# Performance work log

Hardware: AMD Instinct MI355X
Metric: run time of the kernel (lower is better)

## Reference

```python
import jax, jax.numpy as jnp
import numpy as np

N = 30000       # mesh nodes
E = 150000      # mesh edges
L = 128         # latent_size
STEPS = 5       # message_passing_steps
TW = 5          # time_window
TD = 2          # target_dim
NODE_IN = TD + 1 + 9   # u + load + node_type one-hot = 12
EDGE_IN = 2 + 1 + TD   # rel_mesh + dist + grad_u = 5


def _mlp(x, W1, b1, W2, b2, g, be):
    # Linear -> ReLU -> Linear -> ReLU -> LayerNorm (matches MLP module)
    h = jax.nn.relu(x @ W1 + b1)
    h = jax.nn.relu(h @ W2 + b2)
    mu = jnp.mean(h, axis=-1, keepdims=True)
    var = jnp.mean(jnp.square(h - mu), axis=-1, keepdims=True)
    return g * (h - mu) / jnp.sqrt(var + 1e-5) + be


def setup_inputs() -> dict:
    key = jax.random.key(0)
    ks = iter(jax.random.split(key, 64))
    def nrm(shape, s=0.05):
        return jax.random.normal(next(ks), shape, dtype=jnp.float32) * s
    inp = {}
    inp['mesh_pos'] = jax.random.normal(next(ks), (1, N, 2), dtype=jnp.float32)
    inp['node_type'] = jax.random.normal(next(ks), (1, N, 9), dtype=jnp.float32)
    inp['u'] = jax.random.normal(next(ks), (1, N, TD), dtype=jnp.float32)
    inp['load'] = jax.random.normal(next(ks), (1, N, 1), dtype=jnp.float32)
    inp['senders'] = jax.random.randint(next(ks), (E,), 0, N, dtype=jnp.int32)
    inp['receivers'] = jax.random.randint(next(ks), (E,), 0, N, dtype=jnp.int32)
    # node encoder MLP(12 -> 128)
    inp['enc_node_W1'] = nrm((NODE_IN, L)); inp['enc_node_b1'] = nrm((L,), 0.01)
    inp['enc_node_W2'] = nrm((L, L));       inp['enc_node_b2'] = nrm((L,), 0.01)
    inp['enc_node_g'] = jnp.ones((L,), jnp.float32); inp['enc_node_be'] = jnp.zeros((L,), jnp.float32)
    # edge encoder MLP(5 -> 128)
    inp['enc_edge_W1'] = nrm((EDGE_IN, L)); inp['enc_edge_b1'] = nrm((L,), 0.01)
    inp['enc_edge_W2'] = nrm((L, L));       inp['enc_edge_b2'] = nrm((L,), 0.01)
    inp['enc_edge_g'] = jnp.ones((L,), jnp.float32); inp['enc_edge_be'] = jnp.zeros((L,), jnp.float32)
    # STEPS GraphNetBlocks, params stacked along leading axis for lax.scan
    inp['blk_edge_W1'] = nrm((STEPS, 3 * L, L)); inp['blk_edge_b1'] = nrm((STEPS, L), 0.01)
    inp['blk_edge_W2'] = nrm((STEPS, L, L));     inp['blk_edge_b2'] = nrm((STEPS, L), 0.01)
    inp['blk_edge_g'] = jnp.ones((STEPS, L), jnp.float32); inp['blk_edge_be'] = jnp.zeros((STEPS, L), jnp.float32)
    inp['blk_node_W1'] = nrm((STEPS, 2 * L, L)); inp['blk_node_b1'] = nrm((STEPS, L), 0.01)
    inp['blk_node_W2'] = nrm((STEPS, L, L));     inp['blk_node_b2'] = nrm((STEPS, L), 0.01)
    inp['blk_node_g'] = jnp.ones((STEPS, L), jnp.float32); inp['blk_node_be'] = jnp.zeros((STEPS, L), jnp.float32)
    # decoder: Conv1d(L,8,1) -> Swish -> Conv1d(8, TD*TW, 1); kernel-size-1 conv == per-node linear
    inp['dec_W1'] = nrm((L, 8)); inp['dec_b1'] = nrm((8,), 0.01)
    inp['dec_W2'] = nrm((8, TD * TW)); inp['dec_b2'] = nrm((TD * TW,), 0.01)
    return inp


def reference(mesh_pos, node_type, u, load, senders, receivers,
              enc_node_W1, enc_node_b1, enc_node_W2, enc_node_b2, enc_node_g, enc_node_be,
              enc_edge_W1, enc_edge_b1, enc_edge_W2, enc_edge_b2, enc_edge_g, enc_edge_be,
              blk_edge_W1, blk_edge_b1, blk_edge_W2, blk_edge_b2, blk_edge_g, blk_edge_be,
              blk_node_W1, blk_node_b1, blk_node_W2, blk_node_b2, blk_node_g, blk_node_be,
              dec_W1, dec_b1, dec_W2, dec_b2):
    # --- encode ---
    node_feats = jnp.concatenate([u, load, node_type], axis=-1)        # [1,N,12]
    nl = _mlp(node_feats, enc_node_W1, enc_node_b1, enc_node_W2, enc_node_b2, enc_node_g, enc_node_be)
    rel = mesh_pos[:, senders] - mesh_pos[:, receivers]                # [1,E,2]
    dist = jnp.linalg.norm(rel, axis=-1, keepdims=True)                # [1,E,1]
    grad_u = u[:, senders] - u[:, receivers]                           # [1,E,2]
    ef = jnp.concatenate([rel, dist, grad_u], axis=-1)                 # [1,E,5]
    el = _mlp(ef, enc_edge_W1, enc_edge_b1, enc_edge_W2, enc_edge_b2, enc_edge_g, enc_edge_be)
    n_nodes = nl.shape[1]

    # --- process: GraphNetBlocks with residual connections ---
    def block(carry, p):
        nl, el = carry
        edge_in = jnp.concatenate([nl[:, senders], nl[:, receivers], el], axis=-1)  # [1,E,3L]
        ne = _mlp(edge_in, p['eW1'], p['eb1'], p['eW2'], p['eb2'], p['eg'], p['ebe'])
        aggr = jax.vmap(lambda e: jax.ops.segment_sum(e, receivers, num_segments=n_nodes))(ne)  # [1,N,L]
        node_in = jnp.concatenate([nl, aggr], axis=-1)                 # [1,N,2L]
        nn = _mlp(node_in, p['nW1'], p['nb1'], p['nW2'], p['nb2'], p['ng'], p['nbe'])
        return (nl + nn, el + ne), None

    ps = {'eW1': blk_edge_W1, 'eb1': blk_edge_b1, 'eW2': blk_edge_W2, 'eb2': blk_edge_b2,
          'eg': blk_edge_g, 'ebe': blk_edge_be,
          'nW1': blk_node_W1, 'nb1': blk_node_b1, 'nW2': blk_node_W2, 'nb2': blk_node_b2,
          'ng': blk_node_g, 'nbe': blk_node_be}
    (nl, el), _ = jax.lax.scan(block, (nl, el), ps)

    # --- decode (1x1 Conv1d == per-node linear) ---
    h = nl @ dec_W1 + dec_b1
    h = h * jax.nn.sigmoid(h)                                          # Swish(beta=1)
    decoded = h @ dec_W2 + dec_b2                                      # [1,N,TW*TD]
    dt = jnp.repeat(jnp.arange(1, TW + 1, dtype=decoded.dtype), TD)    # [TW*TD]
    delta = (decoded * dt).reshape(-1, TW, TD).transpose(1, 0, 2)      # [TW,N,TD]
    return delta
```

## Files before the change

### kernel.cpp

```cpp
#include <hip/hip_runtime.h>
#include <hip/hip_bf16.h>

#define LNUM 128
#define NNODES 30000
#define NEDGES 150000
#define NSTEPS 5


typedef _Float16 f16;
typedef __attribute__((ext_vector_type(8))) _Float16 f16x8;
typedef __attribute__((ext_vector_type(4))) float f32x4;

__device__ __forceinline__ void glds16(const void* g, void* l) {
    __builtin_amdgcn_global_load_lds(
        (const __attribute__((address_space(1))) void*)g,
        (__attribute__((address_space(3))) void*)l, 16, 0, 0);
}

template<int ROWS, int K, int KP>
__device__ __forceinline__ void mlp_apply(
    const float* __restrict__ xs, float* __restrict__ hv,
    float* __restrict__ mu_s, float* __restrict__ rs_s,
    const float* __restrict__ W1, const float* __restrict__ b1,
    const float* __restrict__ W2, const float* __restrict__ b2,
    const float* __restrict__ g,  const float* __restrict__ be,
    float out[ROWS])
{
    const int t = threadIdx.x;
    float acc[ROWS];
    {
        const float bb = b1[t];
        #pragma unroll
        for (int r = 0; r < ROWS; r++) acc[r] = bb;
    }
    int k = 0;
    for (; k + 4 <= K; k += 4) {
        const float w0 = W1[(k + 0) * LNUM + t];
        const float w1 = W1[(k + 1) * LNUM + t];
        const float w2 = W1[(k + 2) * LNUM + t];
        const float w3 = W1[(k + 3) * LNUM + t];
        #pragma unroll
        for (int r = 0; r < ROWS; r++) {
            const float4 x = *(const float4*)(xs + r * KP + k);
            acc[r] = fmaf(x.x, w0, acc[r]);
            acc[r] = fmaf(x.y, w1, acc[r]);
            acc[r] = fmaf(x.z, w2, acc[r]);
            acc[r] = fmaf(x.w, w3, acc[r]);
        }
    }
    for (; k < K; ++k) {
        const float w = W1[k * LNUM + t];
        #pragma unroll
        for (int r = 0; r < ROWS; r++) acc[r] = fmaf(xs[r * KP + k], w, acc[r]);
    }
    #pragma unroll
    for (int r = 0; r < ROWS; r++) hv[r * LNUM + t] = fmaxf(acc[r], 0.f);
    __syncthreads();
    {
        const float bb = b2[t];
        #pragma unroll
        for (int r = 0; r < ROWS; r++) acc[r] = bb;
    }
    for (int k2 = 0; k2 < LNUM; k2 += 4) {
        const float w0 = W2[(k2 + 0) * LNUM + t];
        const float w1 = W2[(k2 + 1) * LNUM + t];
        const float w2 = W2[(k2 + 2) * LNUM + t];
        const float w3 = W2[(k2 + 3) * LNUM + t];
        #pragma unroll
        for (int r = 0; r < ROWS; r++) {
            const float4 x = *(const float4*)(hv + r * LNUM + k2);
            acc[r] = fmaf(x.x, w0, acc[r]);
            acc[r] = fmaf(x.y, w1, acc[r]);
            acc[r] = fmaf(x.z, w2, acc[r]);
            acc[r] = fmaf(x.w, w3, acc[r]);
        }
    }
    __syncthreads();
    #pragma unroll
    for (int r = 0; r < ROWS; r++) hv[r * LNUM + t] = fmaxf(acc[r], 0.f);
    __syncthreads();
    if (t < ROWS) {
        float s = 0.f, s2 = 0.f;
        for (int kk = 0; kk < LNUM; kk++) {
            const float v = hv[t * LNUM + kk];
            s += v; s2 += v * v;
        }
        const float m = s * (1.0f / LNUM);
        mu_s[t] = m;
        rs_s[t] = rsqrtf(fmaxf(s2 * (1.0f / LNUM) - m * m, 0.f) + 1e-5f);
    }
    __syncthreads();
    const float gg = g[t], bbe = be[t];
    #pragma unroll
    for (int r = 0; r < ROWS; r++)
        out[r] = fmaf(gg * (hv[r * LNUM + t] - mu_s[r]), rs_s[r], bbe);
}

__global__ __launch_bounds__(128) void encode_nodes_k(
    const float* __restrict__ u, const float* __restrict__ load_,
    const float* __restrict__ ntype,
    const float* __restrict__ W1, const float* __restrict__ b1,
    const float* __restrict__ W2, const float* __restrict__ b2,
    const float* __restrict__ g,  const float* __restrict__ be,
    float* __restrict__ nl)
{
    constexpr int ROWS = 4, K = 12, KP = 12;
    __shared__ __align__(16) float xs[ROWS * KP];
    __shared__ __align__(16) float hv[ROWS * LNUM];
    __shared__ float mu_s[ROWS], rs_s[ROWS];
    const int t = threadIdx.x;
    const int base = blockIdx.x * ROWS;
    if (t < ROWS * K) {
        const int r = t / K, k = t % K;
        const int n = base + r;
        float v;
        if (k < 2)      v = u[n * 2 + k];
        else if (k < 3) v = load_[n];
        else            v = ntype[n * 9 + (k - 3)];
        xs[r * KP + k] = v;
    }
    __syncthreads();
    float out[ROWS];
    mlp_apply<ROWS, K, KP>(xs, hv, mu_s, rs_s, W1, b1, W2, b2, g, be, out);
    #pragma unroll
    for (int r = 0; r < ROWS; r++) nl[(base + r) * LNUM + t] = out[r];
}

#define PE1 245760
#define PE2 81920
#define PN1 163840
#define PN2 81920
#define PQ1 4096
#define PQ2 16384
#define PTOT (PE1+PE2+PN1+PN2+PQ1+PQ2)

__global__ __launch_bounds__(256) void prep_w_all_k(
    const float* __restrict__ eW1, const float* __restrict__ eW2,
    const float* __restrict__ nW1, const float* __restrict__ nW2,
    const float* __restrict__ qW1, const float* __restrict__ qW2,
    f16* __restrict__ out)
{
    int j = blockIdx.x * 256 + threadIdx.x;
    if (j >= PTOT) return;
    const float* W; int K, kreal; f16* hi; f16* p = out;
    if (j < PE1) { W = eW1; K = 384; kreal = 384; hi = p; }
    else { p += PE1; j -= PE1;
    if (j < PE2) { W = eW2; K = 128; kreal = 128; hi = p; }
    else { p += PE2; j -= PE2;
    if (j < PN1) { W = nW1; K = 256; kreal = 256; hi = p; }
    else { p += PN1; j -= PN1;
    if (j < PN2) { W = nW2; K = 128; kreal = 128; hi = p; }
    else { p += PN2; j -= PN2;
    if (j < PQ1) { W = qW1; K = 32;  kreal = 5;   hi = p; }
    else { p += PQ1; j -= PQ1;
         { W = qW2; K = 128; kreal = 128; hi = p; } } } } } }
    const int k = j % K;
    const int rem = j / K;
    const int n = rem & 127;
    const int s = rem >> 7;
    const float v = (k < kreal) ? W[((size_t)s * kreal + k) * 128 + n] : 0.f;
    hi[j] = (f16)v;
}

template<int MODE, int NCH1, int K1S>
__global__ __launch_bounds__(256, 5) void mfma_mlp_k(
    const float* __restrict__ in0, const float* __restrict__ in1,
    float* __restrict__ io, float* __restrict__ aggr,
    const int* __restrict__ senders, const int* __restrict__ receivers,
    const f16* __restrict__ W1h, const float* __restrict__ b1,
    const f16* __restrict__ W2h, const float* __restrict__ b2,
    const float* __restrict__ gam, const float* __restrict__ bet,
    int nrows)
{
    __shared__ __align__(16) f16 WH[4096];
    __shared__ __align__(16) unsigned short Yh[64 * 128];

    const int t  = threadIdx.x;
    const int w  = t >> 6;
    const int l  = t & 63;
    const int lr = l & 15;
    const int lg = l >> 4;
    const int swz = lg ^ ((lr >> 1) & 3);
    const int base = blockIdx.x * 64;

    const int eg  = base + w * 16 + lr;
    const int egc = min(eg, nrows - 1);

    int sv = 0, rv = 0;
    if constexpr (MODE != 1) { sv = senders[egc]; rv = receivers[egc]; }

    float feat[8];
    if constexpr (MODE == 2) {
        const float ax = in0[sv * 2], ay = in0[sv * 2 + 1];
        const float bx = in0[rv * 2], by = in0[rv * 2 + 1];
        const float rx = ax - bx, ry = ay - by;
        feat[0] = rx; feat[1] = ry; feat[2] = sqrtf(rx * rx + ry * ry);
        feat[3] = in1[sv * 2] - in1[rv * 2];
        feat[4] = in1[sv * 2 + 1] - in1[rv * 2 + 1];
        feat[5] = 0.f; feat[6] = 0.f; feat[7] = 0.f;
    }

    auto stage = [&](const f16* __restrict__ Wh, const int kst, const int kc) {
        #pragma unroll
        for (int i = 0; i < 2; i++) {
            const int c = 2 * w + i;
            const int ophys = c * 1024 + l * 16;
            const int olog  = ophys ^ (((ophys >> 7) & 3) << 4);
            const int row   = olog >> 6;
            const int slot  = (olog >> 4) & 3;
            glds16(Wh + (size_t)row * kst + kc * 32 + slot * 8, (char*)WH + c * 1024);
        }
    };

    auto gather = [&](int kc, float xv[8]) {
        if constexpr (MODE == 2) {
            #pragma unroll
            for (int j = 0; j < 8; j++) xv[j] = (lg == 0) ? feat[j] : 0.f;
        } else {
            const float* src;
            if constexpr (MODE == 0) {
                if (kc < 4)      src = in0 + (size_t)sv  * 128 + kc * 32 + lg * 8;
                else if (kc < 8) src = in0 + (size_t)rv  * 128 + (kc - 4) * 32 + lg * 8;
                else             src = in1 + (size_t)egc * 128 + (kc - 8) * 32 + lg * 8;
            } else {
                if (kc < 4) src = in0 + (size_t)egc * 128 + kc * 32 + lg * 8;
                else        src = in1 + (size_t)egc * 128 + (kc - 4) * 32 + lg * 8;
            }
            const float4 x0 = *(const float4*)src;
            const float4 x1 = *(const float4*)(src + 4);
            xv[0] = x0.x; xv[1] = x0.y; xv[2] = x0.z; xv[3] = x0.w;
            xv[4] = x1.x; xv[5] = x1.y; xv[6] = x1.z; xv[7] = x1.w;
        }
    };

    const f32x4 zero4 = {0.f, 0.f, 0.f, 0.f};
    f32x4 acc[8];
    #pragma unroll
    for (int mf = 0; mf < 8; mf++) acc[mf] = zero4;

    float xnext[8];
    gather(0, xnext);

    for (int kc = 0; kc < NCH1; ++kc) {
        __syncthreads();
        stage(W1h, K1S, kc);
        union { f16 h[8]; f16x8 v; } XH, XL;
        #pragma unroll
        for (int j = 0; j < 8; j++) {
            const f16 h = (f16)xnext[j];
            XH.h[j] = h;
            XL.h[j] = (f16)(xnext[j] - (float)h);
        }
        __syncthreads();
        if (kc + 1 < NCH1) gather(kc + 1, xnext);
        #pragma unroll
        for (int mf = 0; mf < 8; mf++) {
            const int off = (mf * 16 + lr) * 64 + (swz << 4);
            const f16x8 wh = *(const f16x8*)((const char*)WH + off);
            acc[mf] = __builtin_amdgcn_mfma_f32_16x16x32_f16(XH.v, wh, acc[mf], 0, 0, 0);
            acc[mf] = __builtin_amdgcn_mfma_f32_16x16x32_f16(XL.v, wh, acc[mf], 0, 0, 0);
        }
    }

    #pragma unroll
    for (int mf = 0; mf < 8; mf++) {
        const float bb1 = b1[mf * 16 + lr];
        #pragma unroll
        for (int reg = 0; reg < 4; reg++) {
            float v = acc[mf][reg] + bb1;
            v = fmaxf(v, 0.f);
            union { f16 h; unsigned short u; } cc; cc.h = (f16)v;
            const int row = w * 16 + lg * 4 + reg;
            const int cb  = (mf * 16 + lr) * 2;
            *(unsigned short*)((char*)Yh + row * 256 +
                               (cb ^ (((lg * 4 + reg) & 7) << 4))) = cc.u;
        }
        acc[mf] = zero4;
    }

    for (int kc = 0; kc < 4; ++kc) {
        __syncthreads();
        stage(W2h, 128, kc);
        union { uint4 q; f16x8 v; } YH;
        {
            const int row = w * 16 + lr;
            const int cb  = (kc * 32 + lg * 8) * 2;
            YH.q = *(const uint4*)((const char*)Yh + row * 256 +
                                   (cb ^ ((lr & 7) << 4)));
        }
        __syncthreads();
        #pragma unroll
        for (int mf = 0; mf < 8; mf++) {
            const int off = (mf * 16 + lr) * 64 + (swz << 4);
            const f16x8 wh = *(const f16x8*)((const char*)WH + off);
            acc[mf] = __builtin_amdgcn_mfma_f32_16x16x32_f16(YH.v, wh, acc[mf], 0, 0, 0);
        }
    }

    float vv[8][4];
    float s1[4] = {0, 0, 0, 0}, s2[4] = {0, 0, 0, 0};
    #pragma unroll
    for (int mf = 0; mf < 8; mf++) {
        const float bb2 = b2[mf * 16 + lr];
        #pragma unroll
        for (int reg = 0; reg < 4; reg++) {
            float v = acc[mf][reg] + bb2;
            v = fmaxf(v, 0.f);
            vv[mf][reg] = v;
            s1[reg] += v; s2[reg] += v * v;
        }
    }
    #pragma unroll
    for (int m = 1; m < 16; m <<= 1) {
        #pragma unroll
        for (int reg = 0; reg < 4; reg++) {
            s1[reg] += __shfl_xor(s1[reg], m);
            s2[reg] += __shfl_xor(s2[reg], m);
        }
    }
    float gg[8], b8[8];
    #pragma unroll
    for (int mf = 0; mf < 8; mf++) {
        gg[mf] = gam[mf * 16 + lr];
        b8[mf] = bet[mf * 16 + lr];
    }

    #pragma unroll
    for (int reg = 0; reg < 4; reg++) {
        const float mu = s1[reg] * (1.f / 128.f);
        const float rs = rsqrtf(fmaxf(s2[reg] * (1.f / 128.f) - mu * mu, 0.f) + 1e-5f);
        const int row = w * 16 + lg * 4 + reg;
        const int idx = base + row;
        if (idx < nrows) {
            if constexpr (MODE == 0) {
                const int rc = receivers[idx];
                #pragma unroll
                for (int mf = 0; mf < 8; mf++) {
                    const float o = gg[mf] * (vv[mf][reg] - mu) * rs + b8[mf];
                    atomicAdd(&aggr[(size_t)rc * 128 + mf * 16 + lr], o);
                    io[(size_t)idx * 128 + mf * 16 + lr] += o;
                }
            } else if constexpr (MODE == 1) {
                #pragma unroll
                for (int mf = 0; mf < 8; mf++) {
                    const float o = gg[mf] * (vv[mf][reg] - mu) * rs + b8[mf];
                    io[(size_t)idx * 128 + mf * 16 + lr] += o;
                }
            } else {
                #pragma unroll
                for (int mf = 0; mf < 8; mf++) {
                    const float o = gg[mf] * (vv[mf][reg] - mu) * rs + b8[mf];
                    io[(size_t)idx * 128 + mf * 16 + lr] = o;
                }
            }
        }
    }
}

__global__ __launch_bounds__(128) void decode_k(
    const float* __restrict__ nl,
    const float* __restrict__ W1, const float* __restrict__ b1,
    const float* __restrict__ W2, const float* __restrict__ b2,
    float* __restrict__ out)
{
    constexpr int NPB = 16;
    __shared__ __align__(16) float xs[NPB * LNUM];
    __shared__ float hh[NPB * 8];
    const int t = threadIdx.x;
    const int base = blockIdx.x * NPB;
    for (int r = 0; r < NPB; r++) xs[r * LNUM + t] = nl[(base + r) * LNUM + t];
    __syncthreads();
    {
        const int node = t >> 3, j = t & 7;
        float a = b1[j];
        for (int k = 0; k < LNUM; k++) a = fmaf(xs[node * LNUM + k], W1[k * 8 + j], a);
        hh[node * 8 + j] = a / (1.f + expf(-a));
    }
    __syncthreads();
    for (int idx = t; idx < NPB * 10; idx += 128) {
        const int node = idx / 10, c = idx % 10;
        float a = b2[c];
        #pragma unroll
        for (int j = 0; j < 8; j++) a = fmaf(hh[node * 8 + j], W2[j * 10 + c], a);
        const int tt = c >> 1, d = c & 1;
        out[(size_t)tt * (NNODES * 2) + (size_t)(base + node) * 2 + d] =
            a * (float)(tt + 1);
    }
}

__global__ __launch_bounds__(256) void zero_k(float* __restrict__ p, int n)
{
    const int i = blockIdx.x * 256 + threadIdx.x;
    if (i < n) p[i] = 0.f;
}

extern "C" void kernel_launch(void* const* d_in, const int* in_sizes, int n_in,
                              void* d_out, int out_size, void* d_ws, size_t ws_size,
                              hipStream_t stream) {
    const float* F[34];
    for (int i = 0; i < 34; i++) F[i] = (const float*)d_in[i];
    const int* senders   = (const int*)d_in[4];
    const int* receivers = (const int*)d_in[5];

    const size_t nN = (size_t)NNODES * LNUM;
    const size_t nE = (size_t)NEDGES * LNUM;
    float* nl   = (float*)d_ws;
    float* el   = nl + nN;
    float* aggr = el + nE;
    f16* wb = (f16*)(aggr + nN);
    f16 *eW1h = wb;
    f16 *eW2h = eW1h + PE1;
    f16 *nW1h = eW2h + PE2;
    f16 *nW2h = nW1h + PN1;
    f16 *qW1h = nW2h + PN2;
    f16 *qW2h = qW1h + PQ1;

    prep_w_all_k<<<(PTOT + 255) / 256, 256, 0, stream>>>(
        F[18], F[20], F[24], F[26], F[12], F[14], wb);

    encode_nodes_k<<<NNODES / 4, 128, 0, stream>>>(
        F[2], F[3], F[1], F[6], F[7], F[8], F[9], F[10], F[11], nl);

    const int egrid = (NEDGES + 63) / 64;
    const int ngrid = (NNODES + 63) / 64;

    mfma_mlp_k<2, 1, 32><<<egrid, 256, 0, stream>>>(
        F[0], F[2], el, nullptr, senders, receivers,
        qW1h, F[13], qW2h, F[15], F[16], F[17], NEDGES);

    for (int s = 0; s < NSTEPS; s++) {
        zero_k<<<(NNODES * LNUM + 255) / 256, 256, 0, stream>>>(aggr, NNODES * LNUM);
        mfma_mlp_k<0, 12, 384><<<egrid, 256, 0, stream>>>(
            nl, el, el, aggr, senders, receivers,
            eW1h + (size_t)s * 384 * 128, F[19] + s * LNUM,
            eW2h + (size_t)s * 128 * 128, F[21] + s * LNUM,
            F[22] + s * LNUM, F[23] + s * LNUM, NEDGES);
        mfma_mlp_k<1, 8, 256><<<ngrid, 256, 0, stream>>>(
            nl, aggr, nl, nullptr, nullptr, nullptr,
            nW1h + (size_t)s * 256 * 128, F[25] + s * LNUM,
            nW2h + (size_t)s * 128 * 128, F[27] + s * LNUM,
            F[28] + s * LNUM, F[29] + s * LNUM, NNODES);
    }

    decode_k<<<NNODES / 16, 128, 0, stream>>>(
        nl, F[30], F[31], F[32], F[33], (float*)d_out);
}
```

Measured before the change: 876.5 us.

## Store node and edge latents in fp16 and drop split-precision MFMA for them

```diff
diff --git a/kernel.cpp b/kernel.cpp
--- a/kernel.cpp
+++ b/kernel.cpp
@@ -102,7 +102,7 @@
     const float* __restrict__ W1, const float* __restrict__ b1,
     const float* __restrict__ W2, const float* __restrict__ b2,
     const float* __restrict__ g,  const float* __restrict__ be,
-    float* __restrict__ nl)
+    f16* __restrict__ nl)
 {
     constexpr int ROWS = 4, K = 12, KP = 12;
     __shared__ __align__(16) float xs[ROWS * KP];
@@ -123,7 +123,7 @@
     float out[ROWS];
     mlp_apply<ROWS, K, KP>(xs, hv, mu_s, rs_s, W1, b1, W2, b2, g, be, out);
     #pragma unroll
-    for (int r = 0; r < ROWS; r++) nl[(base + r) * LNUM + t] = out[r];
+    for (int r = 0; r < ROWS; r++) nl[(base + r) * LNUM + t] = (f16)out[r];
 }
 
 #define PE1 245760
@@ -163,9 +163,10 @@
 }
 
 template<int MODE, int NCH1, int K1S>
-__global__ __launch_bounds__(256, 5) void mfma_mlp_k(
-    const float* __restrict__ in0, const float* __restrict__ in1,
-    float* __restrict__ io, float* __restrict__ aggr,
+__global__ __launch_bounds__(256, 6) void mfma_mlp_k(
+    const f16* __restrict__ Lat, const float* __restrict__ Fa,
+    const float* __restrict__ Fb,
+    f16* __restrict__ io, float* __restrict__ aggr,
     const int* __restrict__ senders, const int* __restrict__ receivers,
     const f16* __restrict__ W1h, const float* __restrict__ b1,
     const f16* __restrict__ W2h, const float* __restrict__ b2,
@@ -191,12 +192,12 @@
 
     float feat[8];
     if constexpr (MODE == 2) {
-        const float ax = in0[sv * 2], ay = in0[sv * 2 + 1];
-        const float bx = in0[rv * 2], by = in0[rv * 2 + 1];
+        const float ax = Fa[sv * 2], ay = Fa[sv * 2 + 1];
+        const float bx = Fa[rv * 2], by = Fa[rv * 2 + 1];
         const float rx = ax - bx, ry = ay - by;
         feat[0] = rx; feat[1] = ry; feat[2] = sqrtf(rx * rx + ry * ry);
-        feat[3] = in1[sv * 2] - in1[rv * 2];
-        feat[4] = in1[sv * 2 + 1] - in1[rv * 2 + 1];
+        feat[3] = Fb[sv * 2] - Fb[rv * 2];
+        feat[4] = Fb[sv * 2 + 1] - Fb[rv * 2 + 1];
         feat[5] = 0.f; feat[6] = 0.f; feat[7] = 0.f;
     }
 
@@ -212,24 +213,25 @@
         }
     };
 
-    auto gather = [&](int kc, float xv[8]) {
-        if constexpr (MODE == 2) {
-            #pragma unroll
-            for (int j = 0; j < 8; j++) xv[j] = (lg == 0) ? feat[j] : 0.f;
-        } else {
-            const float* src;
-            if constexpr (MODE == 0) {
-                if (kc < 4)      src = in0 + (size_t)sv  * 128 + kc * 32 + lg * 8;
-                else if (kc < 8) src = in0 + (size_t)rv  * 128 + (kc - 4) * 32 + lg * 8;
-                else             src = in1 + (size_t)egc * 128 + (kc - 8) * 32 + lg * 8;
+    uint4 qn;
+    float xn[8];
+    auto prefetch = [&](int kc) {
+        if constexpr (MODE == 0) {
+            const f16* src;
+            if (kc < 4)      src = Lat + (size_t)sv  * 128 + kc * 32 + lg * 8;
+            else if (kc < 8) src = Lat + (size_t)rv  * 128 + (kc - 4) * 32 + lg * 8;
+            else             src = io  + (size_t)egc * 128 + (kc - 8) * 32 + lg * 8;
+            qn = *(const uint4*)src;
+        } else if constexpr (MODE == 1) {
+            if (kc < 4) {
+                qn = *(const uint4*)(io + (size_t)egc * 128 + kc * 32 + lg * 8);
             } else {
-                if (kc < 4) src = in0 + (size_t)egc * 128 + kc * 32 + lg * 8;
-                else        src = in1 + (size_t)egc * 128 + (kc - 4) * 32 + lg * 8;
+                const float* s = Fa + (size_t)egc * 128 + (kc - 4) * 32 + lg * 8;
+                const float4 a = *(const float4*)s;
+                const float4 b = *(const float4*)(s + 4);
+                xn[0] = a.x; xn[1] = a.y; xn[2] = a.z; xn[3] = a.w;
+                xn[4] = b.x; xn[5] = b.y; xn[6] = b.z; xn[7] = b.w;
             }
-            const float4 x0 = *(const float4*)src;
-            const float4 x1 = *(const float4*)(src + 4);
-            xv[0] = x0.x; xv[1] = x0.y; xv[2] = x0.z; xv[3] = x0.w;
-            xv[4] = x1.x; xv[5] = x1.y; xv[6] = x1.z; xv[7] = x1.w;
         }
     };
 
@@ -238,27 +240,47 @@
     #pragma unroll
     for (int mf = 0; mf < 8; mf++) acc[mf] = zero4;
 
-    float xnext[8];
-    gather(0, xnext);
-
+    prefetch(0);
+
+    #pragma unroll
     for (int kc = 0; kc < NCH1; ++kc) {
         __syncthreads();
         stage(W1h, K1S, kc);
-        union { f16 h[8]; f16x8 v; } XH, XL;
-        #pragma unroll
-        for (int j = 0; j < 8; j++) {
-            const f16 h = (f16)xnext[j];
-            XH.h[j] = h;
-            XL.h[j] = (f16)(xnext[j] - (float)h);
+        const bool isF16 = (MODE == 0) || (MODE == 1 && kc < 4);
+        f16x8 XHv, XLv;
+        bool useXL = false;
+        if constexpr (MODE == 2) {
+            union { f16 h[8]; f16x8 v; } uh, ul;
+            #pragma unroll
+            for (int j = 0; j < 8; j++) {
+                const float x = (lg == 0) ? feat[j] : 0.f;
+                const f16 h = (f16)x;
+                uh.h[j] = h;
+                ul.h[j] = (f16)(x - (float)h);
+            }
+            XHv = uh.v; XLv = ul.v; useXL = true;
+        } else if (isF16) {
+            union { uint4 q; f16x8 v; } cc; cc.q = qn;
+            XHv = cc.v;
+        } else {
+            union { f16 h[8]; f16x8 v; } uh, ul;
+            #pragma unroll
+            for (int j = 0; j < 8; j++) {
+                const f16 h = (f16)xn[j];
+                uh.h[j] = h;
+                ul.h[j] = (f16)(xn[j] - (float)h);
+            }
+            XHv = uh.v; XLv = ul.v; useXL = true;
         }
         __syncthreads();
-        if (kc + 1 < NCH1) gather(kc + 1, xnext);
+        if (kc + 1 < NCH1) prefetch(kc + 1);
         #pragma unroll
         for (int mf = 0; mf < 8; mf++) {
             const int off = (mf * 16 + lr) * 64 + (swz << 4);
             const f16x8 wh = *(const f16x8*)((const char*)WH + off);
-            acc[mf] = __builtin_amdgcn_mfma_f32_16x16x32_f16(XH.v, wh, acc[mf], 0, 0, 0);
-            acc[mf] = __builtin_amdgcn_mfma_f32_16x16x32_f16(XL.v, wh, acc[mf], 0, 0, 0);
+            acc[mf] = __builtin_amdgcn_mfma_f32_16x16x32_f16(XHv, wh, acc[mf], 0, 0, 0);
+            if (useXL)
+                acc[mf] = __builtin_amdgcn_mfma_f32_16x16x32_f16(XLv, wh, acc[mf], 0, 0, 0);
         }
     }
 
@@ -278,6 +300,7 @@
         acc[mf] = zero4;
     }
 
+    #pragma unroll
     for (int kc = 0; kc < 4; ++kc) {
         __syncthreads();
         stage(W2h, 128, kc);
@@ -336,21 +359,26 @@
                 const int rc = receivers[idx];
                 #pragma unroll
                 for (int mf = 0; mf < 8; mf++) {
+                    const int col = mf * 16 + lr;
                     const float o = gg[mf] * (vv[mf][reg] - mu) * rs + b8[mf];
-                    atomicAdd(&aggr[(size_t)rc * 128 + mf * 16 + lr], o);
-                    io[(size_t)idx * 128 + mf * 16 + lr] += o;
+                    atomicAdd(&aggr[(size_t)rc * 128 + col], o);
+                    f16* p = io + (size_t)idx * 128 + col;
+                    *p = (f16)((float)*p + o);
                 }
             } else if constexpr (MODE == 1) {
                 #pragma unroll
                 for (int mf = 0; mf < 8; mf++) {
+                    const int col = mf * 16 + lr;
                     const float o = gg[mf] * (vv[mf][reg] - mu) * rs + b8[mf];
-                    io[(size_t)idx * 128 + mf * 16 + lr] += o;
+                    f16* p = io + (size_t)idx * 128 + col;
+                    *p = (f16)((float)*p + o);
                 }
             } else {
                 #pragma unroll
                 for (int mf = 0; mf < 8; mf++) {
+                    const int col = mf * 16 + lr;
                     const float o = gg[mf] * (vv[mf][reg] - mu) * rs + b8[mf];
-                    io[(size_t)idx * 128 + mf * 16 + lr] = o;
+                    io[(size_t)idx * 128 + col] = (f16)o;
                 }
             }
         }
@@ -358,7 +386,7 @@
 }
 
 __global__ __launch_bounds__(128) void decode_k(
-    const float* __restrict__ nl,
+    const f16* __restrict__ nl,
     const float* __restrict__ W1, const float* __restrict__ b1,
     const float* __restrict__ W2, const float* __restrict__ b2,
     float* __restrict__ out)
@@ -368,7 +396,7 @@
     __shared__ float hh[NPB * 8];
     const int t = threadIdx.x;
     const int base = blockIdx.x * NPB;
-    for (int r = 0; r < NPB; r++) xs[r * LNUM + t] = nl[(base + r) * LNUM + t];
+    for (int r = 0; r < NPB; r++) xs[r * LNUM + t] = (float)nl[(base + r) * LNUM + t];
     __syncthreads();
     {
         const int node = t >> 3, j = t & 7;
@@ -404,9 +432,9 @@
 
     const size_t nN = (size_t)NNODES * LNUM;
     const size_t nE = (size_t)NEDGES * LNUM;
-    float* nl   = (float*)d_ws;
-    float* el   = nl + nN;
-    float* aggr = el + nE;
+    f16* nl16 = (f16*)d_ws;
+    f16* el16 = nl16 + nN;
+    float* aggr = (float*)(el16 + nE);
     f16* wb = (f16*)(aggr + nN);
     f16 *eW1h = wb;
     f16 *eW2h = eW1h + PE1;
@@ -419,29 +447,29 @@
         F[18], F[20], F[24], F[26], F[12], F[14], wb);
 
     encode_nodes_k<<<NNODES / 4, 128, 0, stream>>>(
-        F[2], F[3], F[1], F[6], F[7], F[8], F[9], F[10], F[11], nl);
+        F[2], F[3], F[1], F[6], F[7], F[8], F[9], F[10], F[11], nl16);
 
     const int egrid = (NEDGES + 63) / 64;
     const int ngrid = (NNODES + 63) / 64;
 
     mfma_mlp_k<2, 1, 32><<<egrid, 256, 0, stream>>>(
-        F[0], F[2], el, nullptr, senders, receivers,
+        nullptr, F[0], F[2], el16, nullptr, senders, receivers,
         qW1h, F[13], qW2h, F[15], F[16], F[17], NEDGES);
 
     for (int s = 0; s < NSTEPS; s++) {
         zero_k<<<(NNODES * LNUM + 255) / 256, 256, 0, stream>>>(aggr, NNODES * LNUM);
         mfma_mlp_k<0, 12, 384><<<egrid, 256, 0, stream>>>(
-            nl, el, el, aggr, senders, receivers,
+            nl16, nullptr, nullptr, el16, aggr, senders, receivers,
             eW1h + (size_t)s * 384 * 128, F[19] + s * LNUM,
             eW2h + (size_t)s * 128 * 128, F[21] + s * LNUM,
             F[22] + s * LNUM, F[23] + s * LNUM, NEDGES);
         mfma_mlp_k<1, 8, 256><<<ngrid, 256, 0, stream>>>(
-            nl, aggr, nl, nullptr, nullptr, nullptr,
+            nullptr, aggr, nullptr, nl16, nullptr, nullptr, nullptr,
             nW1h + (size_t)s * 256 * 128, F[25] + s * LNUM,
             nW2h + (size_t)s * 128 * 128, F[27] + s * LNUM,
             F[28] + s * LNUM, F[29] + s * LNUM, NNODES);
     }
 
     decode_k<<<NNODES / 16, 128, 0, stream>>>(
-        nl, F[30], F[31], F[32], F[33], (float*)d_out);
-}
+        nl16, F[30], F[31], F[32], F[33], (float*)d_out);
+}
```

After: 793.7 us. 1.1x faster.
